# Performance work log

Hardware: AMD Instinct MI355X
Metric: run time of the kernel (lower is better)

Reference implementation:

```python
import jax, jax.numpy as jnp
import numpy as np

EPS_SINK = 0.01   # SinkhornDistance eps
N_ITERS = 20      # fixed iteration count (original: max 100 with host-side early exit)
BN_EPS = 1e-5


def _conv(x, w, b):
    # NCHW 3x3 (or 1x1) conv, SAME padding
    y = jax.lax.conv_general_dilated(x, w, (1, 1), 'SAME',
                                     dimension_numbers=('NCHW', 'OIHW', 'NCHW'))
    return y + b[None, :, None, None]


def _bn_train(x, gamma, beta):
    # BatchNorm2d in training mode: batch statistics over (N,H,W)
    m = jnp.mean(x, axis=(0, 2, 3), keepdims=True)
    v = jnp.var(x, axis=(0, 2, 3), keepdims=True)
    return gamma[None, :, None, None] * (x - m) * jax.lax.rsqrt(v + BN_EPS) + beta[None, :, None, None]


def _calc_mean_std(f, eps=1e-5):
    m = jnp.mean(f, axis=(2, 3), keepdims=True)
    s = jnp.sqrt(jnp.var(f, axis=(2, 3), keepdims=True) + eps)
    return m, s


def _sinkhorn_pi(x, y, eps):
    # x: [b, n, d] content points, y: [b, m, d] style points. Cosine-distance cost.
    xn = x / jnp.linalg.norm(x, axis=-1, keepdims=True)
    yn = y / jnp.linalg.norm(y, axis=-1, keepdims=True)
    C = 1.0 - jnp.einsum('bnd,bmd->bnm', xn, yn)          # [b, n, m]
    b, n, m = C.shape
    log_mu = jnp.log(jnp.full((b, n), 1.0 / n) + 1e-8)
    log_nu = jnp.log(jnp.full((b, m), 1.0 / m) + 1e-8)

    def Mmat(u, v):
        # (-C + u_i + v_j) / eps
        return (-C + u[..., None] + v[..., None, :]) / eps

    def step(carry, _):
        u, v = carry
        u = eps * (log_mu - jax.scipy.special.logsumexp(Mmat(u, v), axis=-1)) + u
        v = eps * (log_nu - jax.scipy.special.logsumexp(Mmat(u, v), axis=-2)) + v
        return (u, v), None

    (u, v), _ = jax.lax.scan(step, (jnp.zeros((b, n)), jnp.zeros((b, m))), None, length=N_ITERS)
    return jnp.exp(Mmat(u, v))                             # transport plan pi


def setup_inputs() -> dict:
    key = jax.random.key(0)
    ks = jax.random.split(key, 16)
    bs, dim, h, w = 4, 512, 32, 32
    s = 0.05
    return {
        'content_feat': jax.random.normal(ks[0], (bs, dim, h, w), jnp.float32),
        'style_feat':   jax.random.normal(ks[1], (bs, dim, h, w), jnp.float32),
        # alpha_predictor (version 1): conv(1024->256,3x3) ReLU BN, conv(256->256,3x3) ReLU BN, conv(256->512,3x3)
        'w1': jax.random.normal(ks[2], (256, 1024, 3, 3), jnp.float32) * s,
        'b1': jnp.zeros((256,), jnp.float32),
        'g1': jnp.ones((256,), jnp.float32),
        'be1': jnp.zeros((256,), jnp.float32),
        'w2': jax.random.normal(ks[3], (256, 256, 3, 3), jnp.float32) * s,
        'b2': jnp.zeros((256,), jnp.float32),
        'g2': jnp.ones((256,), jnp.float32),
        'be2': jnp.zeros((256,), jnp.float32),
        'w3': jax.random.normal(ks[4], (512, 256, 3, 3), jnp.float32) * s,
        'b3': jnp.zeros((512,), jnp.float32),
        # stand-in decoder head: 3x3 conv 512->3 (decoder is an external injected module)
        'dec_w': jax.random.normal(ks[5], (3, 512, 3, 3), jnp.float32) * s,
        'dec_b': jnp.zeros((3,), jnp.float32),
    }


def reference(content_feat, style_feat, w1, b1, g1, be1, w2, b2, g2, be2, w3, b3, dec_w, dec_b):
    bs, dim, h, w = content_feat.shape
    cf = content_feat.reshape(bs, dim, h * w).transpose(0, 2, 1)   # [b, hw, d]
    sf = style_feat.reshape(bs, dim, h * w).transpose(0, 2, 1)
    pi = _sinkhorn_pi(cf, sf, EPS_SINK) * (h * w)                  # style_assign: pi * h * w
    t = jnp.einsum('bnm,bmd->bnd', pi, sf).transpose(0, 2, 1).reshape(bs, dim, h, w)
    cm, cs = _calc_mean_std(content_feat)
    c_normed = (content_feat - cm) / cs
    a = _bn_train(jax.nn.relu(_conv(jnp.concatenate([t, content_feat], axis=1), w1, b1)), g1, be1)
    a = _bn_train(jax.nn.relu(_conv(a, w2, b2)), g2, be2)
    alpha = _conv(a, w3, b3)
    t = alpha * c_normed + t
    g_t = _conv(t, dec_w, dec_b)
    return g_t
```

## Files before the change

### kernel.cpp

```cpp
#include <hip/hip_runtime.h>

typedef unsigned short u16;
typedef unsigned int u32;
typedef unsigned long long u64;
typedef float f32x4 __attribute__((ext_vector_type(4)));
typedef short bf16x8 __attribute__((ext_vector_type(8)));

#define DEV static __device__ __forceinline__

DEV float bf2f(u16 u){ union{float f; u32 i;} x; x.i = ((u32)u) << 16; return x.f; }
DEV u16 f2bf(float f){ union{float f; u32 i;} x; x.f = f; u32 u = x.i;
  return (u16)((u + 0x7fffu + ((u >> 16) & 1u)) >> 16); }
DEV u16 f2h(float f){ _Float16 h = (_Float16)f; u16 u; __builtin_memcpy(&u, &h, 2); return u; }
DEV float h2f(u16 u){ _Float16 h; __builtin_memcpy(&h, &u, 2); return (float)h; }
DEV uint4 pack8(const u16* s){ uint4 v;
  v.x = (u32)s[0] | ((u32)s[1]<<16); v.y = (u32)s[2] | ((u32)s[3]<<16);
  v.z = (u32)s[4] | ((u32)s[5]<<16); v.w = (u32)s[6] | ((u32)s[7]<<16); return v; }
DEV f32x4 mfma16(bf16x8 a, bf16x8 b, f32x4 c){
  return __builtin_amdgcn_mfma_f32_16x16x32_bf16(a, b, c, 0, 0, 0);
}
DEV bf16x8 ldfrag(const u16* p){ return *(const bf16x8*)p; }

DEV void st_agent(float* p, float v){
  __hip_atomic_store(p, v, __ATOMIC_RELAXED, __HIP_MEMORY_SCOPE_AGENT); }
DEV float2 ld_agent2(const float* p){
  u64 u = __hip_atomic_load((const u64*)p, __ATOMIC_RELAXED, __HIP_MEMORY_SCOPE_AGENT);
  union{u64 u; float2 f;} c; c.u = u; return c.f; }
DEV void st_agent_u32(u32* p, u32 v){
  __hip_atomic_store(p, v, __ATOMIC_RELAXED, __HIP_MEMORY_SCOPE_AGENT); }
DEV u32 ld_agent_u32(const u32* p){
  return __hip_atomic_load(p, __ATOMIC_RELAXED, __HIP_MEMORY_SCOPE_AGENT); }

constexpr float SCL = 144.269504088896341f;
constexpr float LOG2MU = -9.99998522680257f;

constexpr size_t MB = 1ull << 20;
constexpr size_t OFF_G    = 0;
constexpr size_t OFF_GT   = 8*MB;
constexpr size_t OFF_U    = 16*MB;
constexpr size_t OFF_V    = OFF_U   + (16<<10);
constexpr size_t OFF_BAR  = OFF_V   + (16<<10);
constexpr size_t OFF_INS  = OFF_BAR + (16<<10);
constexpr size_t OFF_CNM  = OFF_INS + (16<<10);
constexpr size_t OFF_CNIS = OFF_CNM + (8<<10);
constexpr size_t OFF_BNS  = OFF_CNIS+ (8<<10);
constexpr size_t OFF_PNP  = OFF_BNS + (4<<10);
constexpr size_t OFF_CFH  = 17*MB;
constexpr size_t OFF_CFL  = 21*MB;
constexpr size_t OFF_SFH  = 25*MB;
constexpr size_t OFF_SFL  = 29*MB;
constexpr size_t OFF_SNB  = 33*MB;
constexpr size_t OFF_TN   = 37*MB;
constexpr size_t OFF_TCP  = 45*MB;
constexpr size_t OFF_W1P  = 53*MB;
constexpr size_t OFF_W2P  = OFF_W1P + 9*256*1024*2;
constexpr size_t OFF_W3P  = OFF_W2P + 9*256*256*2;
constexpr size_t OFF_WDP  = OFF_W3P + 9*512*256*2;
constexpr size_t OFF_PIP  = 62*MB;
constexpr size_t OFF_Z1  = 17*MB;
constexpr size_t OFF_A1P = 25*MB;
constexpr size_t OFF_Z2  = 27*MB;
constexpr size_t OFF_A2P = 35*MB;
constexpr size_t OFF_T2P = 17*MB;

__global__ void stats_k(const float* __restrict__ cf, const float* __restrict__ sf,
                        float* __restrict__ cnm, float* __restrict__ cnis,
                        float* __restrict__ part, float* __restrict__ zUV,
                        float* __restrict__ zBNS, u32* __restrict__ zbar,
                        const float* __restrict__ w1, const float* __restrict__ w2,
                        const float* __restrict__ w3, const float* __restrict__ wd,
                        u16* __restrict__ w1p, u16* __restrict__ w2p,
                        u16* __restrict__ w3p, u16* __restrict__ wdp){
  int blk = blockIdx.x;
  if (blk < 2048){
    int bd = blk;
    float4 v = ((const float4*)(cf + (size_t)bd*1024))[threadIdx.x];
    float s = v.x+v.y+v.z+v.w;
    float q = v.x*v.x+v.y*v.y+v.z*v.z+v.w*v.w;
    #pragma unroll
    for (int m = 32; m >= 1; m >>= 1){ s += __shfl_xor(s, m, 64); q += __shfl_xor(q, m, 64); }
    __shared__ float ls[4], lq[4];
    int w = threadIdx.x >> 6;
    if ((threadIdx.x & 63) == 0){ ls[w] = s; lq[w] = q; }
    __syncthreads();
    if (threadIdx.x == 0){
      float S = ls[0]+ls[1]+ls[2]+ls[3], Q = lq[0]+lq[1]+lq[2]+lq[3];
      float mean = S * (1.f/1024.f);
      float var  = Q * (1.f/1024.f) - mean*mean;
      cnm[bd] = mean; cnis[bd] = rsqrtf(var + 1e-5f);
    }
    return;
  }
  if (blk < 2304){
    int rel = blk - 2048;
    int x = rel & 15, y = (rel >> 4) & 7, src = rel >> 7;
    const float* in = src ? sf : cf;
    int p = x*256 + threadIdx.x;
    int b = p >> 10, pp = p & 1023;
    const float* base = in + ((size_t)(b*512 + y*64))*1024 + pp;
    float s = 0.f;
    #pragma unroll 8
    for (int d = 0; d < 64; ++d){ float xx = base[(size_t)d*1024]; s += xx*xx; }
    part[((size_t)(src*8 + y))*4096 + p] = s;
    return;
  }
  if (blk < 2336){
    zUV[(blk - 2304)*256 + threadIdx.x] = 0.f;
    return;
  }
  if (blk < 2340){
    zBNS[(blk - 2336)*256 + threadIdx.x] = 0.f;
    return;
  }
  if (blk < 2356){
    zbar[(blk - 2340)*256 + threadIdx.x] = 0u;
    return;
  }
  int pblk = blk - 2356;
  const float* w; u16* wp; int CI, NCK, rel;
  if (pblk < 512){ w = w1; wp = w1p; CI = 1024; NCK = 32; rel = pblk; }
  else if (pblk < 640){ w = w2; wp = w2p; CI = 256; NCK = 8; rel = pblk - 512; }
  else if (pblk < 896){ w = w3; wp = w3p; CI = 256; NCK = 8; rel = pblk - 640; }
  else {
    int o = (pblk - 896)*256 + threadIdx.x;
    int ci = o & 511; int r = o >> 9; int co = r & 15; int tap = r >> 4;
    wdp[o] = f2bf((co < 3) ? wd[(size_t)(co*512 + ci)*9 + tap] : 0.f);
    return;
  }
  int g = rel / NCK, ck = rel % NCK;
  __shared__ float L[16*288];
  const float* base = w + ((size_t)(g*16)*CI + ck*32)*9;
  #pragma unroll
  for (int i = 0; i < 18; ++i){
    int idx = i*256 + threadIdx.x;
    int row = idx / 288, col = idx - row*288;
    L[row*288 + col] = base[(size_t)row*CI*9 + col];
  }
  __syncthreads();
  u16* dst = wp + ((size_t)(g*NCK + ck)*9)*512;
  #pragma unroll
  for (int i = 0; i < 18; ++i){
    int j = i*256 + threadIdx.x;
    int tap = j >> 9, r = j & 511, lane = r >> 3, e = r & 7;
    int co = lane & 15, cil = ((lane >> 4) & 3)*8 + e;
    dst[j] = f2bf(L[co*288 + cil*9 + tap]);
  }
}

__global__ void tsplit_k(const float* __restrict__ cf, const float* __restrict__ sf,
                         const float* __restrict__ pnp,
                         u16* __restrict__ cfh, u16* __restrict__ cfl,
                         u16* __restrict__ sfh, u16* __restrict__ sfl,
                         u16* __restrict__ tcp, u16* __restrict__ snb){
  __shared__ float tile[64][65];
  int z = blockIdx.z, is_style = z >> 2, b = z & 3;
  const float* src = is_style ? sf : cf;
  u16* hi = is_style ? sfh : cfh;
  u16* lo = is_style ? sfl : cfl;
  int p0 = blockIdx.x*64, d0 = blockIdx.y*64;
  int r = threadIdx.x >> 2, c0 = (threadIdx.x & 3) * 16;
  const float* sp = src + ((size_t)(b*512 + d0 + r))*1024 + p0 + c0;
  float v[16];
  #pragma unroll
  for (int e = 0; e < 4; ++e){
    float4 t4 = ((const float4*)sp)[e];
    v[e*4+0]=t4.x; v[e*4+1]=t4.y; v[e*4+2]=t4.z; v[e*4+3]=t4.w;
  }
  #pragma unroll
  for (int j = 0; j < 16; ++j) tile[r][c0+j] = v[j];
  if (is_style){
    u16 t16[16];
    #pragma unroll
    for (int j = 0; j < 16; ++j) t16[j] = f2bf(v[j]);
    uint4* ap = (uint4*)(snb + ((size_t)(b*512 + d0 + r))*1024 + p0 + c0);
    ap[0] = pack8(t16); ap[1] = pack8(t16+8);
  }
  __syncthreads();
  int pr = r, dc0 = c0;
  float inv;
  {
    const float* pp = pnp + (size_t)(is_style ? 8*4096 : 0) + ((b<<10) + p0 + pr);
    float s = 0.f;
    #pragma unroll
    for (int j = 0; j < 8; ++j) s += pp[j*4096];
    inv = rsqrtf(s);
  }
  u16 h16[16], l16[16], t16[16];
  #pragma unroll
  for (int j = 0; j < 16; ++j){
    float x = tile[dc0+j][pr];
    t16[j] = f2bf(x);
    float xn = x * inv;
    u16 h = f2bf(xn);
    h16[j] = h;
    l16[j] = f2bf(xn - bf2f(h));
  }
  size_t orow = (size_t)((b<<10) + p0 + pr);
  uint4* hp = (uint4*)(hi + orow*512 + d0 + dc0);
  uint4* lp = (uint4*)(lo + orow*512 + d0 + dc0);
  hp[0] = pack8(h16); hp[1] = pack8(h16+8);
  lp[0] = pack8(l16); lp[1] = pack8(l16+8);
  if (!is_style){
    int D = d0 + dc0;
    size_t off = ((size_t)(16 + (D>>5))*4096 + orow)*32 + (D&31);
    *(uint4*)(tcp + off)     = pack8(t16);
    *(uint4*)(tcp + off + 8) = pack8(t16+8);
  }
}

__global__ __launch_bounds__(256) void cgemm_k(const u16* __restrict__ cfh, const u16* __restrict__ cfl,
        const u16* __restrict__ sfh, const u16* __restrict__ sfl,
        u16* __restrict__ G, u16* __restrict__ Gt){
  __shared__ __align__(16) u16 SH[4*128*40];
  u16* Ah = SH;          u16* Al = SH + 5120;
  u16* Bh = SH + 10240;  u16* Bl = SH + 15360;
  int b = blockIdx.z;
  size_t abase = ((size_t)((b<<10) + blockIdx.x*128))*512;
  size_t bbase = ((size_t)((b<<10) + blockIdx.y*128))*512;
  int lane = threadIdx.x & 63, wid = threadIdx.x >> 6;
  int wm = (wid >> 1)*64, wn = (wid & 1)*64;
  int fr = lane & 15, qd = lane >> 4;
  int sr = threadIdx.x >> 1, sc = (threadIdx.x & 1)*16;
  const u16 *pA = cfh + abase, *pB = cfl + abase, *pC = sfh + bbase, *pD = sfl + bbase;
  uint4 rA0, rA1, rB0, rB1, rC0, rC1, rD0, rD1;
  auto issue = [&](int kk){
    size_t g0 = (size_t)sr*512 + kk + sc;
    rA0 = *(const uint4*)(pA + g0); rA1 = *(const uint4*)(pA + g0 + 8);
    rB0 = *(const uint4*)(pB + g0); rB1 = *(const uint4*)(pB + g0 + 8);
    rC0 = *(const uint4*)(pC + g0); rC1 = *(const uint4*)(pC + g0 + 8);
    rD0 = *(const uint4*)(pD + g0); rD1 = *(const uint4*)(pD + g0 + 8);
  };
  f32x4 acc[4][4] = {};
  issue(0);
  for (int kk = 0; kk < 512; kk += 32){
    *(uint4*)&Ah[sr*40+sc]   = rA0; *(uint4*)&Ah[sr*40+sc+8] = rA1;
    *(uint4*)&Al[sr*40+sc]   = rB0; *(uint4*)&Al[sr*40+sc+8] = rB1;
    *(uint4*)&Bh[sr*40+sc]   = rC0; *(uint4*)&Bh[sr*40+sc+8] = rC1;
    *(uint4*)&Bl[sr*40+sc]   = rD0; *(uint4*)&Bl[sr*40+sc+8] = rD1;
    __syncthreads();
    if (kk + 32 < 512) issue(kk + 32);
    bf16x8 bhf[4], blf[4];
    #pragma unroll
    for (int ni = 0; ni < 4; ++ni){
      bhf[ni] = ldfrag(&Bh[(wn + ni*16 + fr)*40 + qd*8]);
      blf[ni] = ldfrag(&Bl[(wn + ni*16 + fr)*40 + qd*8]);
    }
    #pragma unroll
    for (int mi = 0; mi < 4; ++mi){
      bf16x8 ah = ldfrag(&Ah[(wm + mi*16 + fr)*40 + qd*8]);
      bf16x8 al = ldfrag(&Al[(wm + mi*16 + fr)*40 + qd*8]);
      #pragma unroll
      for (int ni = 0; ni < 4; ++ni){
        acc[mi][ni] = mfma16(ah, bhf[ni], acc[mi][ni]);
        acc[mi][ni] = mfma16(ah, blf[ni], acc[mi][ni]);
        acc[mi][ni] = mfma16(al, bhf[ni], acc[mi][ni]);
      }
    }
    __syncthreads();
  }
  #pragma unroll
  for (int mi = 0; mi < 4; ++mi)
    #pragma unroll
    for (int ni = 0; ni < 4; ++ni)
      #pragma unroll
      for (int rg = 0; rg < 4; ++rg){
        int r = wm + mi*16 + qd*4 + rg;
        int c = wn + ni*16 + fr;
        SH[r*136 + c] = f2h((acc[mi][ni][rg] - 1.f) * SCL);
      }
  __syncthreads();
  size_t gb = (((size_t)b) << 20) + (size_t)(blockIdx.x*128)*1024 + blockIdx.y*128;
  #pragma unroll
  for (int i = 0; i < 8; ++i){
    int idx = i*256 + threadIdx.x;
    int r = idx >> 4, c4 = idx & 15;
    *(uint4*)(G + gb + (size_t)r*1024 + c4*8) = *(const uint4*)&SH[r*136 + c4*8];
  }
  __syncthreads();
  #pragma unroll
  for (int mi = 0; mi < 4; ++mi)
    #pragma unroll
    for (int ni = 0; ni < 4; ++ni)
      #pragma unroll
      for (int rg = 0; rg < 4; ++rg){
        int r = wm + mi*16 + qd*4 + rg;
        int c = wn + ni*16 + fr;
        SH[c*136 + r] = f2h((acc[mi][ni][rg] - 1.f) * SCL);
      }
  __syncthreads();
  size_t gtb = (((size_t)b) << 20) + (size_t)(blockIdx.y*128)*1024 + blockIdx.x*128;
  #pragma unroll
  for (int i = 0; i < 8; ++i){
    int idx = i*256 + threadIdx.x;
    int r = idx >> 4, c4 = idx & 15;
    *(uint4*)(Gt + gtb + (size_t)r*1024 + c4*8) = *(const uint4*)&SH[r*136 + c4*8];
  }
}

__global__ __launch_bounds__(512) void sink_k(const u16* __restrict__ G, const u16* __restrict__ Gt,
        float* __restrict__ U, float* __restrict__ V,
        u32* __restrict__ flags, u16* __restrict__ pip,
        const u16* __restrict__ cin, const u16* __restrict__ wpk,
        float* __restrict__ z1out){
  __shared__ __align__(16) u16 LL[2][16*1024];
  int blk = blockIdx.x;
  int tid = threadIdx.x;
  if (blk >= 256){
    u16* As = LL[0];
    int cbid = blk - 256;
    int cx = cbid & 15, cy = (cbid >> 4) & 3, b = cbid >> 6;
    const int NCK_TOT = 32, NCK = 16, ck0 = 16;
    int c0 = cy*64, r0 = cx*2;
    int lane = tid & 63, wid = tid >> 6;
    int wm = (wid >> 2)*32, wn = (wid & 3)*16;
    int fr = lane & 15, qd = lane >> 4;
    int hrow = tid >> 2, ah = (tid & 3)*8;
    int gy = r0 - 1 + (hrow >> 5);
    bool a_ok = ((unsigned)gy < 32u);
    size_t arow = (size_t)(b<<10) + (r0-1)*32 + hrow;
    uint4 pa = {0,0,0,0};
    auto issueA = [&](int ck){
      if (a_ok) pa = *(const uint4*)(cin + ((size_t)(ck0+ck)*4096 + arow)*32 + ah);
    };
    int g0 = (c0 + wn) >> 4;
    const u16* wb = wpk + ((size_t)g0*NCK_TOT + ck0)*9*512 + lane*8;
    f32x4 acc[2] = {};
    issueA(0);
    for (int ck = 0; ck < NCK; ++ck){
      *(uint4*)&As[hrow*40 + ah] = pa;
      __syncthreads();
      if (ck + 1 < NCK) issueA(ck + 1);
      #pragma unroll
      for (int tap = 0; tap < 9; ++tap){
        const int dy = tap/3 - 1, dx = tap%3 - 1;
        bf16x8 bf = ldfrag(wb + (size_t)(ck*9 + tap)*512);
        #pragma unroll
        for (int mi = 0; mi < 2; ++mi){
          int p0w = wm + mi*16;
          int pcol = (p0w & 31) + fr + dx;
          int lr = (p0w >> 5) + dy + 1;
          bool okc = (unsigned)pcol < 32u;
          bf16x8 af = ldfrag(&As[(lr*32 + (okc ? pcol : 0))*40 + qd*8]);
          if (!okc) af = bf16x8(0);
          acc[mi] = mfma16(af, bf, acc[mi]);
        }
      }
      __syncthreads();
    }
    #pragma unroll
    for (int mi = 0; mi < 2; ++mi)
      #pragma unroll
      for (int rg = 0; rg < 4; ++rg){
        int pp = cx*64 + wm + mi*16 + qd*4 + rg;
        int cc = c0 + wn + fr;
        size_t ro = (size_t)((b<<10) + pp);
        z1out[(size_t)4096*256 + ro*256 + cc] = acc[mi][rg];
      }
    return;
  }
  int b = blk >> 6;
  int sub = blk & 63;
  int rb = sub << 4;
  size_t gbase = ((size_t)((b << 10) + rb)) << 10;
  {
    const uint4* g0 = (const uint4*)(G + gbase);
    const uint4* g1 = (const uint4*)(Gt + gbase);
    uint4* d0 = (uint4*)LL[0];
    uint4* d1 = (uint4*)LL[1];
    #pragma unroll
    for (int i = 0; i < 4; ++i){
      d0[i*512 + tid] = g0[i*512 + tid];
      d1[i*512 + tid] = g1[i*512 + tid];
    }
  }
  __syncthreads();
  int wid = tid >> 6, lane = tid & 63;
  float* Ub = U + (b << 10);
  float* Vb = V + (b << 10);
  u32* fgrp = flags + (b << 6)*16;
  u32* fmine = fgrp + sub*16;
  int r0 = wid << 1;
  int cbase = lane << 2;
  int budget = 1 << 21;

  float o0 = 0.f, o1 = 0.f;
  auto dopass = [&](int which, const float* __restrict__ inv, float* __restrict__ outv, int tgt){
    float va[16];
    #pragma unroll
    for (int k = 0; k < 4; ++k){
      #pragma unroll
      for (int j = 0; j < 2; ++j){
        float2 t = ld_agent2(inv + k*256 + cbase + j*2);
        va[k*4 + j*2]     = t.x;
        va[k*4 + j*2 + 1] = t.y;
      }
    }
    #pragma unroll
    for (int rr = 0; rr < 2; ++rr){
      int row = r0 + rr;
      float x[16]; float mx = -3.0e38f;
      #pragma unroll
      for (int k = 0; k < 4; ++k){
        uint2 g2 = *(const uint2*)(&LL[which][row*1024 + k*256 + cbase]);
        float t0 = h2f((u16)(g2.x & 0xffffu)) + va[k*4+0];
        float t1 = h2f((u16)(g2.x >> 16))     + va[k*4+1];
        float t2 = h2f((u16)(g2.y & 0xffffu)) + va[k*4+2];
        float t3 = h2f((u16)(g2.y >> 16))     + va[k*4+3];
        x[k*4+0]=t0; x[k*4+1]=t1; x[k*4+2]=t2; x[k*4+3]=t3;
        mx = fmaxf(mx, fmaxf(fmaxf(t0,t1), fmaxf(t2,t3)));
      }
      #pragma unroll
      for (int m = 32; m >= 1; m >>= 1) mx = fmaxf(mx, __shfl_xor(mx, m, 64));
      float s = 0.f;
      #pragma unroll
      for (int i = 0; i < 16; ++i) s += exp2f(x[i] - mx);
      #pragma unroll
      for (int m = 32; m >= 1; m >>= 1) s += __shfl_xor(s, m, 64);
      float o = LOG2MU - (mx + log2f(s));
      if (rr == 0) o0 = o; else o1 = o;
      if (lane == 0) st_agent(outv + rb + row, o);
    }
    __syncthreads();
    if (tid == 0) st_agent_u32(fmine, (u32)tgt);
    if (tid < 64){
      u32* fl = fgrp + tid*16;
      for (;;){
        u32 v = ld_agent_u32(fl);
        if (__all((int)(v >= (u32)tgt))) break;
        if (--budget < 0) break;
        __builtin_amdgcn_s_sleep(1);
      }
    }
    __syncthreads();
  };

  float ku0 = 0.f, ku1 = 0.f;
  for (int it = 0; it < 20; ++it){
    dopass(0, Vb, Ub, 2*it + 1);
    ku0 = o0; ku1 = o1;
    dopass(1, Ub, Vb, 2*it + 2);
  }

  float va[16];
  #pragma unroll
  for (int k = 0; k < 4; ++k){
    #pragma unroll
    for (int j = 0; j < 2; ++j){
      float2 t = ld_agent2(Vb + k*256 + cbase + j*2);
      va[k*4 + j*2]     = t.x;
      va[k*4 + j*2 + 1] = t.y;
    }
  }
  #pragma unroll
  for (int rr = 0; rr < 2; ++rr){
    int row = r0 + rr;
    float ur = (rr == 0 ? ku0 : ku1) + 10.f;
    size_t orow = ((size_t)((b << 10) + rb + row)) << 10;
    #pragma unroll
    for (int k = 0; k < 4; ++k){
      uint2 g2 = *(const uint2*)(&LL[0][row*1024 + k*256 + cbase]);
      u16 o[4];
      o[0] = f2bf(exp2f(h2f((u16)(g2.x & 0xffffu)) + va[k*4+0] + ur));
      o[1] = f2bf(exp2f(h2f((u16)(g2.x >> 16))     + va[k*4+1] + ur));
      o[2] = f2bf(exp2f(h2f((u16)(g2.y & 0xffffu)) + va[k*4+2] + ur));
      o[3] = f2bf(exp2f(h2f((u16)(g2.y >> 16))     + va[k*4+3] + ur));
      uint2 pk; pk.x = (u32)o[0] | ((u32)o[1]<<16); pk.y = (u32)o[2] | ((u32)o[3]<<16);
      *(uint2*)(pip + orow + k*256 + cbase) = pk;
    }
  }
}

__global__ __launch_bounds__(256) void tgemm_k(const u16* __restrict__ pip,
        const u16* __restrict__ snb, float* __restrict__ tn, u16* __restrict__ tcp){
  __shared__ __align__(16) u16 As[64*40], Bs[128*40];
  int b = blockIdx.z, p0 = blockIdx.x*64, d0 = blockIdx.y*128;
  int tid = threadIdx.x, lane = tid & 63, wid = tid >> 6;
  int wm = (wid >> 1)*32, wn = (wid & 1)*64;
  int fr = lane & 15, qd = lane >> 4;
  int a_r = tid >> 2, a_c = (tid & 3)*8;
  int b_r = tid >> 1, b_c = (tid & 1)*16;
  const u16* Arow = pip + (((size_t)((b<<10) + p0 + a_r)) << 10) + a_c;
  const u16* Brow = snb + (((size_t)(b*512 + d0 + b_r)) << 10) + b_c;
  uint4 pa, pb0, pb1;
  auto issue = [&](int kk){
    pa = *(const uint4*)(Arow + kk);
    const uint4* bp = (const uint4*)(Brow + kk);
    pb0 = bp[0]; pb1 = bp[1];
  };
  f32x4 acc[2][4] = {};
  issue(0);
  for (int kk = 0; kk < 1024; kk += 32){
    *(uint4*)&As[a_r*40 + a_c] = pa;
    *(uint4*)&Bs[b_r*40 + b_c] = pb0;
    *(uint4*)&Bs[b_r*40 + b_c + 8] = pb1;
    __syncthreads();
    if (kk + 32 < 1024) issue(kk + 32);
    bf16x8 bfr[4];
    #pragma unroll
    for (int ni = 0; ni < 4; ++ni) bfr[ni] = ldfrag(&Bs[(wn + ni*16 + fr)*40 + qd*8]);
    #pragma unroll
    for (int mi = 0; mi < 2; ++mi){
      bf16x8 afr = ldfrag(&As[(wm + mi*16 + fr)*40 + qd*8]);
      #pragma unroll
      for (int ni = 0; ni < 4; ++ni) acc[mi][ni] = mfma16(afr, bfr[ni], acc[mi][ni]);
    }
    __syncthreads();
  }
  #pragma unroll
  for (int mi = 0; mi < 2; ++mi)
    #pragma unroll
    for (int ni = 0; ni < 4; ++ni)
      #pragma unroll
      for (int rg = 0; rg < 4; ++rg){
        int p = p0 + wm + mi*16 + qd*4 + rg;
        int d = d0 + wn + ni*16 + fr;
        float vout = acc[mi][ni][rg];
        size_t ro = (size_t)((b<<10) + p);
        tn[ro*512 + d] = vout;
        tcp[((size_t)(d>>5)*4096 + ro)*32 + (d&31)] = f2bf(vout);
      }
}

template<int CI, int CO, int KSPLIT, int MODE>
__global__ __launch_bounds__(256) void conv_k(const u16* __restrict__ inp, const u16* __restrict__ wpk,
        const float* __restrict__ bias, float* __restrict__ fout, u16* __restrict__ bout,
        const u16* __restrict__ tcp, const float* __restrict__ cnm, const float* __restrict__ cnis,
        const float* __restrict__ tn){
  constexpr int NCK_TOT = CI/32, NCK = NCK_TOT/KSPLIT;
  __shared__ __align__(16) u16 As[128*40];
  int b = blockIdx.z & 3, ks = blockIdx.z >> 2;
  int c0 = blockIdx.y*64;
  int r0 = blockIdx.x*2;
  int tid = threadIdx.x, lane = tid & 63, wid = tid >> 6;
  int wm = (wid >> 1)*32, wn = (wid & 1)*32;
  int fr = lane & 15, qd = lane >> 4;
  int ck0 = ks*NCK;
  int hrow = tid >> 1;
  int ah = (tid & 1)*16;
  int gy = r0 - 1 + (hrow >> 5);
  bool a_ok = ((unsigned)gy < 32u);
  size_t arow = (size_t)(b<<10) + (r0-1)*32 + hrow;
  uint4 pa0 = {0,0,0,0}, pa1 = {0,0,0,0};
  auto issueA = [&](int ck){
    if (a_ok){
      const uint4* s = (const uint4*)(inp + ((size_t)(ck0+ck)*4096 + arow)*32 + ah);
      pa0 = s[0]; pa1 = s[1];
    }
  };
  int g0 = (c0 + wn) >> 4;
  const u16* wb0 = wpk + ((size_t)(g0    )*NCK_TOT + ck0)*9*512 + lane*8;
  const u16* wb1 = wpk + ((size_t)(g0 + 1)*NCK_TOT + ck0)*9*512 + lane*8;

  f32x4 acc[2][2] = {};
  issueA(0);
  for (int ck = 0; ck < NCK; ++ck){
    *(uint4*)&As[hrow*40 + ah]     = pa0;
    *(uint4*)&As[hrow*40 + ah + 8] = pa1;
    __syncthreads();
    if (ck + 1 < NCK) issueA(ck + 1);
    #pragma unroll
    for (int tap = 0; tap < 9; ++tap){
      const int dy = tap/3 - 1, dx = tap%3 - 1;
      bf16x8 bf0 = ldfrag(wb0 + (size_t)(ck*9 + tap)*512);
      bf16x8 bf1 = ldfrag(wb1 + (size_t)(ck*9 + tap)*512);
      #pragma unroll
      for (int mi = 0; mi < 2; ++mi){
        int p0w = wm + mi*16;
        int pcol = (p0w & 31) + fr + dx;
        int lr = (p0w >> 5) + dy + 1;
        bool okc = (unsigned)pcol < 32u;
        bf16x8 af = ldfrag(&As[(lr*32 + (okc ? pcol : 0))*40 + qd*8]);
        if (!okc) af = bf16x8(0);
        acc[mi][0] = mfma16(af, bf0, acc[mi][0]);
        acc[mi][1] = mfma16(af, bf1, acc[mi][1]);
      }
    }
    __syncthreads();
  }
  #pragma unroll
  for (int mi = 0; mi < 2; ++mi)
    #pragma unroll
    for (int ni = 0; ni < 2; ++ni)
      #pragma unroll
      for (int rg = 0; rg < 4; ++rg){
        int pp = blockIdx.x*64 + wm + mi*16 + qd*4 + rg;
        int cc = c0 + wn + ni*16 + fr;
        float v = acc[mi][ni][rg];
        size_t ro = (size_t)((b<<10) + pp);
        if (MODE == 0){
          fout[(size_t)ks*4096*CO + ro*CO + cc] = v;
        } else {
          float alpha = v + bias[cc];
          float cn = (bf2f(tcp[((size_t)(16 + (cc>>5))*4096 + ro)*32 + (cc&31)])
                      - cnm[(b<<9) + cc]) * cnis[(b<<9) + cc];
          bout[((size_t)(cc>>5)*4096 + ro)*32 + (cc&31)] = f2bf(alpha*cn + tn[ro*512 + cc]);
        }
      }
}

__global__ __launch_bounds__(512) void dec_k(const u16* __restrict__ t2p, const u16* __restrict__ wdp,
                                             const float* __restrict__ db, float* __restrict__ out){
  __shared__ float wlds[3*4608];
  int tid = threadIdx.x;
  for (int k = tid; k < 3*4608; k += 512){
    int c = k / 4608, rem = k - c*4608;
    int tap = rem >> 9, ci = rem & 511;
    wlds[k] = bf2f(wdp[(size_t)(tap*16 + c)*512 + ci]);
  }
  __syncthreads();
  int b = blockIdx.x >> 5;
  int p = ((blockIdx.x & 31) << 5) + (tid >> 4);
  int sub = tid & 15;
  int py = p >> 5, px = p & 31;
  float a0 = 0.f, a1 = 0.f, a2 = 0.f;
  for (int tap = 0; tap < 9; ++tap){
    int sy = py + tap/3 - 1, sx = px + tap%3 - 1;
    if (((unsigned)sy < 32u) && ((unsigned)sx < 32u)){
      size_t row = (size_t)((b<<10) + (sy<<5) + sx);
      const float* w0 = wlds + tap*512;
      #pragma unroll
      for (int j = 0; j < 4; ++j){
        int ci0 = j*128 + sub*8;
        uint4 v = *(const uint4*)(t2p + ((size_t)(ci0>>5)*4096 + row)*32 + (ci0&31));
        u32 ww[4] = {v.x, v.y, v.z, v.w};
        #pragma unroll
        for (int e = 0; e < 8; ++e){
          float x = bf2f((u16)((e & 1) ? (ww[e>>1] >> 16) : (ww[e>>1] & 0xffffu)));
          a0 += x * w0[ci0 + e];
          a1 += x * w0[4608 + ci0 + e];
          a2 += x * w0[9216 + ci0 + e];
        }
      }
    }
  }
  #pragma unroll
  for (int m = 8; m >= 1; m >>= 1){
    a0 += __shfl_xor(a0, m, 64);
    a1 += __shfl_xor(a1, m, 64);
    a2 += __shfl_xor(a2, m, 64);
  }
  if (sub == 0){
    out[((size_t)(b*3 + 0) << 10) + p] = a0 + db[0];
    out[((size_t)(b*3 + 1) << 10) + p] = a1 + db[1];
    out[((size_t)(b*3 + 2) << 10) + p] = a2 + db[2];
  }
}

__global__ void bn_stats_k(const float* __restrict__ z, const float* __restrict__ bias,
                           float* __restrict__ sums){
  int c = blockIdx.x*64 + (threadIdx.x & 63);
  int w = threadIdx.x >> 6;
  int rbase = blockIdx.y*128 + w*32;
  float bi = bias[c];
  float s = 0.f, q = 0.f;
  for (int i = 0; i < 32; ++i){
    size_t ro = (size_t)(rbase + i)*256 + c;
    float x = fmaxf(z[ro] + z[4096*256 + ro] + bi, 0.f);
    s += x; q += x*x;
  }
  __shared__ float ls[4][64], lq[4][64];
  ls[w][threadIdx.x & 63] = s; lq[w][threadIdx.x & 63] = q;
  __syncthreads();
  if (threadIdx.x < 64){
    float S = ls[0][threadIdx.x]+ls[1][threadIdx.x]+ls[2][threadIdx.x]+ls[3][threadIdx.x];
    float Q = lq[0][threadIdx.x]+lq[1][threadIdx.x]+lq[2][threadIdx.x]+lq[3][threadIdx.x];
    atomicAdd(&sums[blockIdx.x*64 + threadIdx.x], S);
    atomicAdd(&sums[256 + blockIdx.x*64 + threadIdx.x], Q);
  }
}

__global__ void bn_apply_k(const float* __restrict__ z, const float* __restrict__ bias,
                           const float* __restrict__ sums, const float* __restrict__ gamma,
                           const float* __restrict__ beta, u16* __restrict__ ap){
  int idx = blockIdx.x*256 + threadIdx.x;
  float4 va = ((const float4*)z)[idx];
  float4 vb = ((const float4*)(z + 4096*256))[idx];
  int row = idx >> 6;
  int cc0 = (idx << 2) & 255;
  float e[4] = {va.x+vb.x, va.y+vb.y, va.z+vb.z, va.w+vb.w};
  u16 o[4];
  #pragma unroll
  for (int k = 0; k < 4; ++k){
    int c = cc0 + k;
    float mean = sums[c] * (1.f/4096.f);
    float var  = sums[256 + c] * (1.f/4096.f) - mean*mean;
    float sc = gamma[c] * rsqrtf(var + 1e-5f);
    float sh = beta[c] - mean*sc;
    float x = fmaxf(e[k] + bias[c], 0.f);
    o[k] = f2bf(x*sc + sh);
  }
  uint2 pk; pk.x = (u32)o[0] | ((u32)o[1]<<16); pk.y = (u32)o[2] | ((u32)o[3]<<16);
  *(uint2*)(ap + ((size_t)(cc0>>5)*4096 + row)*32 + (cc0&31)) = pk;
}

extern "C" void kernel_launch(void* const* d_in, const int* in_sizes, int n_in,
                              void* d_out, int out_size, void* d_ws, size_t ws_size,
                              hipStream_t stream){
  const float* cf  = (const float*)d_in[0];
  const float* sf  = (const float*)d_in[1];
  const float* w1  = (const float*)d_in[2];
  const float* b1  = (const float*)d_in[3];
  const float* g1  = (const float*)d_in[4];
  const float* be1 = (const float*)d_in[5];
  const float* w2  = (const float*)d_in[6];
  const float* b2  = (const float*)d_in[7];
  const float* g2  = (const float*)d_in[8];
  const float* be2 = (const float*)d_in[9];
  const float* w3  = (const float*)d_in[10];
  const float* b3  = (const float*)d_in[11];
  const float* dw  = (const float*)d_in[12];
  const float* db  = (const float*)d_in[13];

  char* ws = (char*)d_ws;
  u16* G    = (u16*)(ws + OFF_G);
  u16* Gt   = (u16*)(ws + OFF_GT);
  float* U    = (float*)(ws + OFF_U);
  float* V    = (float*)(ws + OFF_V);
  u32* bar    = (u32*)(ws + OFF_BAR);
  float* cnm  = (float*)(ws + OFF_CNM);
  float* cnis = (float*)(ws + OFF_CNIS);
  float* bns1 = (float*)(ws + OFF_BNS);
  float* bns2 = bns1 + 512;
  float* pnp  = (float*)(ws + OFF_PNP);
  u16* cfh = (u16*)(ws + OFF_CFH);
  u16* cfl = (u16*)(ws + OFF_CFL);
  u16* sfh = (u16*)(ws + OFF_SFH);
  u16* sfl = (u16*)(ws + OFF_SFL);
  u16* snb = (u16*)(ws + OFF_SNB);
  float* tn  = (float*)(ws + OFF_TN);
  u16* tcp = (u16*)(ws + OFF_TCP);
  u16* w1p = (u16*)(ws + OFF_W1P);
  u16* w2p = (u16*)(ws + OFF_W2P);
  u16* w3p = (u16*)(ws + OFF_W3P);
  u16* wdp = (u16*)(ws + OFF_WDP);
  u16* pip = (u16*)(ws + OFF_PIP);
  float* z1  = (float*)(ws + OFF_Z1);
  u16*   a1p = (u16*)(ws + OFF_A1P);
  float* z2  = (float*)(ws + OFF_Z2);
  u16*   a2p = (u16*)(ws + OFF_A2P);
  u16*   t2p = (u16*)(ws + OFF_T2P);

  stats_k<<<3540, 256, 0, stream>>>(cf, sf, cnm, cnis, pnp, U, bns1, bar,
                                    w1, w2, w3, dw, w1p, w2p, w3p, wdp);
  tsplit_k<<<dim3(16, 8, 8), 256, 0, stream>>>(cf, sf, pnp, cfh, cfl, sfh, sfl, tcp, snb);

  cgemm_k<<<dim3(8, 8, 4), 256, 0, stream>>>(cfh, cfl, sfh, sfl, G, Gt);

  sink_k<<<512, 512, 0, stream>>>(G, Gt, U, V, bar, pip, tcp, w1p, z1);

  tgemm_k<<<dim3(16, 4, 4), 256, 0, stream>>>(pip, snb, tn, tcp);

  conv_k<1024, 256, 2, 0><<<dim3(16, 4, 4), 256, 0, stream>>>(
      tcp, w1p, nullptr, z1, nullptr, nullptr, nullptr, nullptr, nullptr);
  bn_stats_k<<<dim3(4, 32), 256, 0, stream>>>(z1, b1, bns1);
  bn_apply_k<<<1024, 256, 0, stream>>>(z1, b1, bns1, g1, be1, a1p);

  conv_k<256, 256, 2, 0><<<dim3(16, 4, 8), 256, 0, stream>>>(
      a1p, w2p, nullptr, z2, nullptr, nullptr, nullptr, nullptr, nullptr);
  bn_stats_k<<<dim3(4, 32), 256, 0, stream>>>(z2, b2, bns2);
  bn_apply_k<<<1024, 256, 0, stream>>>(z2, b2, bns2, g2, be2, a2p);

  conv_k<256, 512, 1, 1><<<dim3(16, 8, 4), 256, 0, stream>>>(
      a2p, w3p, b3, nullptr, t2p, tcp, cnm, cnis, tn);

  dec_k<<<128, 512, 0, stream>>>(t2p, wdp, db, (float*)d_out);

  (void)in_sizes; (void)n_in; (void)out_size; (void)ws_size;
}
```

Measured before the change: 389.9 us.

## Fuse transport GEMM into Sinkhorn kernel and merge BN stats/apply with grid barrier

After: 400.4 us. 1.03x slower.

```diff
diff --git a/kernel.cpp b/kernel.cpp
--- a/kernel.cpp
+++ b/kernel.cpp
@@ -23,6 +23,8 @@
 
 DEV void st_agent(float* p, float v){
   __hip_atomic_store(p, v, __ATOMIC_RELAXED, __HIP_MEMORY_SCOPE_AGENT); }
+DEV float ld_agentf(const float* p){
+  return __hip_atomic_load(p, __ATOMIC_RELAXED, __HIP_MEMORY_SCOPE_AGENT); }
 DEV float2 ld_agent2(const float* p){
   u64 u = __hip_atomic_load((const u64*)p, __ATOMIC_RELAXED, __HIP_MEMORY_SCOPE_AGENT);
   union{u64 u; float2 f;} c; c.u = u; return c.f; }
@@ -40,8 +42,8 @@
 constexpr size_t OFF_U    = 16*MB;
 constexpr size_t OFF_V    = OFF_U   + (16<<10);
 constexpr size_t OFF_BAR  = OFF_V   + (16<<10);
-constexpr size_t OFF_INS  = OFF_BAR + (16<<10);
-constexpr size_t OFF_CNM  = OFF_INS + (16<<10);
+constexpr size_t OFF_CTR  = OFF_BAR + (16<<10);
+constexpr size_t OFF_CNM  = OFF_CTR + (16<<10);
 constexpr size_t OFF_CNIS = OFF_CNM + (8<<10);
 constexpr size_t OFF_BNS  = OFF_CNIS+ (8<<10);
 constexpr size_t OFF_PNP  = OFF_BNS + (4<<10);
@@ -56,7 +58,6 @@
 constexpr size_t OFF_W2P  = OFF_W1P + 9*256*1024*2;
 constexpr size_t OFF_W3P  = OFF_W2P + 9*256*256*2;
 constexpr size_t OFF_WDP  = OFF_W3P + 9*512*256*2;
-constexpr size_t OFF_PIP  = 62*MB;
 constexpr size_t OFF_Z1  = 17*MB;
 constexpr size_t OFF_A1P = 25*MB;
 constexpr size_t OFF_Z2  = 27*MB;
@@ -67,6 +68,7 @@
                         float* __restrict__ cnm, float* __restrict__ cnis,
                         float* __restrict__ part, float* __restrict__ zUV,
                         float* __restrict__ zBNS, u32* __restrict__ zbar,
+                        u32* __restrict__ zctr,
                         const float* __restrict__ w1, const float* __restrict__ w2,
                         const float* __restrict__ w3, const float* __restrict__ wd,
                         u16* __restrict__ w1p, u16* __restrict__ w2p,
@@ -116,7 +118,11 @@
     zbar[(blk - 2340)*256 + threadIdx.x] = 0u;
     return;
   }
-  int pblk = blk - 2356;
+  if (blk < 2357){
+    zctr[threadIdx.x] = 0u;
+    return;
+  }
+  int pblk = blk - 2357;
   const float* w; u16* wp; int CI, NCK, rel;
   if (pblk < 512){ w = w1; wp = w1p; CI = 1024; NCK = 32; rel = pblk; }
   else if (pblk < 640){ w = w2; wp = w2p; CI = 256; NCK = 8; rel = pblk - 512; }
@@ -299,9 +305,10 @@
 
 __global__ __launch_bounds__(512) void sink_k(const u16* __restrict__ G, const u16* __restrict__ Gt,
         float* __restrict__ U, float* __restrict__ V,
-        u32* __restrict__ flags, u16* __restrict__ pip,
+        u32* __restrict__ flags,
         const u16* __restrict__ cin, const u16* __restrict__ wpk,
-        float* __restrict__ z1out){
+        float* __restrict__ z1out,
+        const u16* __restrict__ snb, float* __restrict__ tn, u16* __restrict__ tcp){
   __shared__ __align__(16) u16 LL[2][16*1024];
   int blk = blockIdx.x;
   int tid = threadIdx.x;
@@ -375,6 +382,7 @@
   }
   __syncthreads();
   int wid = tid >> 6, lane = tid & 63;
+  int fr = lane & 15, qd = lane >> 4;
   float* Ub = U + (b << 10);
   float* Vb = V + (b << 10);
   u32* fgrp = flags + (b << 6)*16;
@@ -441,84 +449,72 @@
     dopass(1, Ub, Vb, 2*it + 2);
   }
 
-  float va[16];
-  #pragma unroll
-  for (int k = 0; k < 4; ++k){
-    #pragma unroll
-    for (int j = 0; j < 2; ++j){
-      float2 t = ld_agent2(Vb + k*256 + cbase + j*2);
-      va[k*4 + j*2]     = t.x;
-      va[k*4 + j*2 + 1] = t.y;
-    }
-  }
-  #pragma unroll
-  for (int rr = 0; rr < 2; ++rr){
-    int row = r0 + rr;
-    float ur = (rr == 0 ? ku0 : ku1) + 10.f;
-    size_t orow = ((size_t)((b << 10) + rb + row)) << 10;
+  {
+    float va[16];
     #pragma unroll
     for (int k = 0; k < 4; ++k){
-      uint2 g2 = *(const uint2*)(&LL[0][row*1024 + k*256 + cbase]);
-      u16 o[4];
-      o[0] = f2bf(exp2f(h2f((u16)(g2.x & 0xffffu)) + va[k*4+0] + ur));
-      o[1] = f2bf(exp2f(h2f((u16)(g2.x >> 16))     + va[k*4+1] + ur));
-      o[2] = f2bf(exp2f(h2f((u16)(g2.y & 0xffffu)) + va[k*4+2] + ur));
-      o[3] = f2bf(exp2f(h2f((u16)(g2.y >> 16))     + va[k*4+3] + ur));
-      uint2 pk; pk.x = (u32)o[0] | ((u32)o[1]<<16); pk.y = (u32)o[2] | ((u32)o[3]<<16);
-      *(uint2*)(pip + orow + k*256 + cbase) = pk;
-    }
-  }
-}
-
-__global__ __launch_bounds__(256) void tgemm_k(const u16* __restrict__ pip,
-        const u16* __restrict__ snb, float* __restrict__ tn, u16* __restrict__ tcp){
-  __shared__ __align__(16) u16 As[64*40], Bs[128*40];
-  int b = blockIdx.z, p0 = blockIdx.x*64, d0 = blockIdx.y*128;
-  int tid = threadIdx.x, lane = tid & 63, wid = tid >> 6;
-  int wm = (wid >> 1)*32, wn = (wid & 1)*64;
-  int fr = lane & 15, qd = lane >> 4;
-  int a_r = tid >> 2, a_c = (tid & 3)*8;
-  int b_r = tid >> 1, b_c = (tid & 1)*16;
-  const u16* Arow = pip + (((size_t)((b<<10) + p0 + a_r)) << 10) + a_c;
-  const u16* Brow = snb + (((size_t)(b*512 + d0 + b_r)) << 10) + b_c;
-  uint4 pa, pb0, pb1;
-  auto issue = [&](int kk){
-    pa = *(const uint4*)(Arow + kk);
-    const uint4* bp = (const uint4*)(Brow + kk);
-    pb0 = bp[0]; pb1 = bp[1];
-  };
-  f32x4 acc[2][4] = {};
-  issue(0);
-  for (int kk = 0; kk < 1024; kk += 32){
-    *(uint4*)&As[a_r*40 + a_c] = pa;
-    *(uint4*)&Bs[b_r*40 + b_c] = pb0;
-    *(uint4*)&Bs[b_r*40 + b_c + 8] = pb1;
-    __syncthreads();
-    if (kk + 32 < 1024) issue(kk + 32);
-    bf16x8 bfr[4];
-    #pragma unroll
-    for (int ni = 0; ni < 4; ++ni) bfr[ni] = ldfrag(&Bs[(wn + ni*16 + fr)*40 + qd*8]);
-    #pragma unroll
-    for (int mi = 0; mi < 2; ++mi){
-      bf16x8 afr = ldfrag(&As[(wm + mi*16 + fr)*40 + qd*8]);
-      #pragma unroll
-      for (int ni = 0; ni < 4; ++ni) acc[mi][ni] = mfma16(afr, bfr[ni], acc[mi][ni]);
-    }
-    __syncthreads();
-  }
-  #pragma unroll
-  for (int mi = 0; mi < 2; ++mi)
-    #pragma unroll
-    for (int ni = 0; ni < 4; ++ni)
+      #pragma unroll
+      for (int j = 0; j < 2; ++j){
+        float2 t = ld_agent2(Vb + k*256 + cbase + j*2);
+        va[k*4 + j*2]     = t.x;
+        va[k*4 + j*2 + 1] = t.y;
+      }
+    }
+    #pragma unroll
+    for (int rr = 0; rr < 2; ++rr){
+      int row = r0 + rr;
+      float ur = (rr == 0 ? ku0 : ku1) + 10.f;
+      int sw = (row & 7) << 3;
+      #pragma unroll
+      for (int k = 0; k < 4; ++k){
+        uint2 g2 = *(const uint2*)(&LL[0][row*1024 + k*256 + cbase]);
+        u16 o[4];
+        o[0] = f2bf(exp2f(h2f((u16)(g2.x & 0xffffu)) + va[k*4+0] + ur));
+        o[1] = f2bf(exp2f(h2f((u16)(g2.x >> 16))     + va[k*4+1] + ur));
+        o[2] = f2bf(exp2f(h2f((u16)(g2.y & 0xffffu)) + va[k*4+2] + ur));
+        o[3] = f2bf(exp2f(h2f((u16)(g2.y >> 16))     + va[k*4+3] + ur));
+        uint2 pk; pk.x = (u32)o[0] | ((u32)o[1]<<16); pk.y = (u32)o[2] | ((u32)o[3]<<16);
+        *(uint2*)(&LL[1][row*1024 + ((k*256 + cbase) ^ sw)]) = pk;
+      }
+    }
+  }
+  __syncthreads();
+  {
+    int d0w = wid << 6;
+    const u16* Bb = snb + (((size_t)(b*512 + d0w)) << 10);
+    f32x4 tac[4] = {};
+    uint4 pb0, pb1, pb2, pb3;
+    auto issueB = [&](int ks){
+      int off = ks*32 + qd*8;
+      pb0 = *(const uint4*)(Bb + (((size_t)(     fr)) << 10) + off);
+      pb1 = *(const uint4*)(Bb + (((size_t)(16 + fr)) << 10) + off);
+      pb2 = *(const uint4*)(Bb + (((size_t)(32 + fr)) << 10) + off);
+      pb3 = *(const uint4*)(Bb + (((size_t)(48 + fr)) << 10) + off);
+    };
+    issueB(0);
+    int asw = (fr & 7) << 3;
+    for (int ks = 0; ks < 32; ++ks){
+      union{uint4 u; bf16x8 v;} c0_, c1_, c2_, c3_;
+      c0_.u = pb0; c1_.u = pb1; c2_.u = pb2; c3_.u = pb3;
+      if (ks + 1 < 32) issueB(ks + 1);
+      bf16x8 af = ldfrag(&LL[1][fr*1024 + ((ks*32 + qd*8) ^ asw)]);
+      tac[0] = mfma16(af, c0_.v, tac[0]);
+      tac[1] = mfma16(af, c1_.v, tac[1]);
+      tac[2] = mfma16(af, c2_.v, tac[2]);
+      tac[3] = mfma16(af, c3_.v, tac[3]);
+    }
+    #pragma unroll
+    for (int t = 0; t < 4; ++t)
       #pragma unroll
       for (int rg = 0; rg < 4; ++rg){
-        int p = p0 + wm + mi*16 + qd*4 + rg;
-        int d = d0 + wn + ni*16 + fr;
-        float vout = acc[mi][ni][rg];
-        size_t ro = (size_t)((b<<10) + p);
-        tn[ro*512 + d] = vout;
-        tcp[((size_t)(d>>5)*4096 + ro)*32 + (d&31)] = f2bf(vout);
-      }
+        int p = qd*4 + rg;
+        int d = d0w + t*16 + fr;
+        size_t ro = (size_t)((b<<10) + rb + p);
+        float v = tac[t][rg];
+        tn[ro*512 + d] = v;
+        tcp[((size_t)(d>>5)*4096 + ro)*32 + (d&31)] = f2bf(v);
+      }
+  }
 }
 
 template<int CI, int CO, int KSPLIT, int MODE>
@@ -646,51 +642,39 @@
   }
 }
 
-__global__ void bn_stats_k(const float* __restrict__ z, const float* __restrict__ bias,
-                           float* __restrict__ sums){
-  int c = blockIdx.x*64 + (threadIdx.x & 63);
-  int w = threadIdx.x >> 6;
-  int rbase = blockIdx.y*128 + w*32;
+__global__ __launch_bounds__(256) void bn_k(const float* __restrict__ z, const float* __restrict__ bias,
+                    float* __restrict__ sums, const float* __restrict__ gamma,
+                    const float* __restrict__ beta, u16* __restrict__ ap,
+                    u32* __restrict__ ctr){
+  int c = threadIdx.x;
+  int r0 = blockIdx.x*32;
   float bi = bias[c];
+  float xv[32];
   float s = 0.f, q = 0.f;
+  #pragma unroll
   for (int i = 0; i < 32; ++i){
-    size_t ro = (size_t)(rbase + i)*256 + c;
-    float x = fmaxf(z[ro] + z[4096*256 + ro] + bi, 0.f);
-    s += x; q += x*x;
-  }
-  __shared__ float ls[4][64], lq[4][64];
-  ls[w][threadIdx.x & 63] = s; lq[w][threadIdx.x & 63] = q;
-  __syncthreads();
-  if (threadIdx.x < 64){
-    float S = ls[0][threadIdx.x]+ls[1][threadIdx.x]+ls[2][threadIdx.x]+ls[3][threadIdx.x];
-    float Q = lq[0][threadIdx.x]+lq[1][threadIdx.x]+lq[2][threadIdx.x]+lq[3][threadIdx.x];
-    atomicAdd(&sums[blockIdx.x*64 + threadIdx.x], S);
-    atomicAdd(&sums[256 + blockIdx.x*64 + threadIdx.x], Q);
-  }
-}
-
-__global__ void bn_apply_k(const float* __restrict__ z, const float* __restrict__ bias,
-                           const float* __restrict__ sums, const float* __restrict__ gamma,
-                           const float* __restrict__ beta, u16* __restrict__ ap){
-  int idx = blockIdx.x*256 + threadIdx.x;
-  float4 va = ((const float4*)z)[idx];
-  float4 vb = ((const float4*)(z + 4096*256))[idx];
-  int row = idx >> 6;
-  int cc0 = (idx << 2) & 255;
-  float e[4] = {va.x+vb.x, va.y+vb.y, va.z+vb.z, va.w+vb.w};
-  u16 o[4];
-  #pragma unroll
-  for (int k = 0; k < 4; ++k){
-    int c = cc0 + k;
-    float mean = sums[c] * (1.f/4096.f);
-    float var  = sums[256 + c] * (1.f/4096.f) - mean*mean;
-    float sc = gamma[c] * rsqrtf(var + 1e-5f);
-    float sh = beta[c] - mean*sc;
-    float x = fmaxf(e[k] + bias[c], 0.f);
-    o[k] = f2bf(x*sc + sh);
-  }
-  uint2 pk; pk.x = (u32)o[0] | ((u32)o[1]<<16); pk.y = (u32)o[2] | ((u32)o[3]<<16);
-  *(uint2*)(ap + ((size_t)(cc0>>5)*4096 + row)*32 + (cc0&31)) = pk;
+    size_t ro = (size_t)(r0 + i)*256 + c;
+    float x = fmaxf(z[ro] + z[(size_t)4096*256 + ro] + bi, 0.f);
+    xv[i] = x; s += x; q += x*x;
+  }
+  atomicAdd(&sums[c], s);
+  atomicAdd(&sums[256 + c], q);
+  __syncthreads();
+  if (c == 0){
+    __hip_atomic_fetch_add(ctr, 1u, __ATOMIC_RELAXED, __HIP_MEMORY_SCOPE_AGENT);
+    int budget = 1 << 21;
+    while (ld_agent_u32(ctr) < 128u && --budget > 0) __builtin_amdgcn_s_sleep(1);
+  }
+  __syncthreads();
+  float S = ld_agentf(&sums[c]), Q = ld_agentf(&sums[256 + c]);
+  float mean = S * (1.f/4096.f);
+  float var  = Q * (1.f/4096.f) - mean*mean;
+  float sc = gamma[c] * rsqrtf(var + 1e-5f);
+  float sh = beta[c] - mean*sc;
+  u16* apc = ap + ((size_t)(c>>5)*4096)*32 + (c&31);
+  #pragma unroll
+  for (int i = 0; i < 32; ++i)
+    apc[(size_t)(r0 + i)*32] = f2bf(xv[i]*sc + sh);
 }
 
 extern "C" void kernel_launch(void* const* d_in, const int* in_sizes, int n_in,
@@ -717,6 +701,7 @@
   float* U    = (float*)(ws + OFF_U);
   float* V    = (float*)(ws + OFF_V);
   u32* bar    = (u32*)(ws + OFF_BAR);
+  u32* ctr    = (u32*)(ws + OFF_CTR);
   float* cnm  = (float*)(ws + OFF_CNM);
   float* cnis = (float*)(ws + OFF_CNIS);
   float* bns1 = (float*)(ws + OFF_BNS);
@@ -733,32 +718,27 @@
   u16* w2p = (u16*)(ws + OFF_W2P);
   u16* w3p = (u16*)(ws + OFF_W3P);
   u16* wdp = (u16*)(ws + OFF_WDP);
-  u16* pip = (u16*)(ws + OFF_PIP);
   float* z1  = (float*)(ws + OFF_Z1);
   u16*   a1p = (u16*)(ws + OFF_A1P);
   float* z2  = (float*)(ws + OFF_Z2);
   u16*   a2p = (u16*)(ws + OFF_A2P);
   u16*   t2p = (u16*)(ws + OFF_T2P);
 
-  stats_k<<<3540, 256, 0, stream>>>(cf, sf, cnm, cnis, pnp, U, bns1, bar,
+  stats_k<<<3541, 256, 0, stream>>>(cf, sf, cnm, cnis, pnp, U, bns1, bar, ctr,
                                     w1, w2, w3, dw, w1p, w2p, w3p, wdp);
   tsplit_k<<<dim3(16, 8, 8), 256, 0, stream>>>(cf, sf, pnp, cfh, cfl, sfh, sfl, tcp, snb);
 
   cgemm_k<<<dim3(8, 8, 4), 256, 0, stream>>>(cfh, cfl, sfh, sfl, G, Gt);
 
-  sink_k<<<512, 512, 0, stream>>>(G, Gt, U, V, bar, pip, tcp, w1p, z1);
-
-  tgemm_k<<<dim3(16, 4, 4), 256, 0, stream>>>(pip, snb, tn, tcp);
+  sink_k<<<512, 512, 0, stream>>>(G, Gt, U, V, bar, tcp, w1p, z1, snb, tn, tcp);
 
   conv_k<1024, 256, 2, 0><<<dim3(16, 4, 4), 256, 0, stream>>>(
       tcp, w1p, nullptr, z1, nullptr, nullptr, nullptr, nullptr, nullptr);
-  bn_stats_k<<<dim3(4, 32), 256, 0, stream>>>(z1, b1, bns1);
-  bn_apply_k<<<1024, 256, 0, stream>>>(z1, b1, bns1, g1, be1, a1p);
+  bn_k<<<128, 256, 0, stream>>>(z1, b1, bns1, g1, be1, a1p, ctr);
 
   conv_k<256, 256, 2, 0><<<dim3(16, 4, 8), 256, 0, stream>>>(
       a1p, w2p, nullptr, z2, nullptr, nullptr, nullptr, nullptr, nullptr);
-  bn_stats_k<<<dim3(4, 32), 256, 0, stream>>>(z2, b2, bns2);
-  bn_apply_k<<<1024, 256, 0, stream>>>(z2, b2, bns2, g2, be2, a2p);
+  bn_k<<<128, 256, 0, stream>>>(z2, b2, bns2, g2, be2, a2p, ctr + 16);
 
   conv_k<256, 512, 1, 1><<<dim3(16, 8, 4), 256, 0, stream>>>(
       a2p, w3p, b3, nullptr, t2p, tcp, cnm, cnis, tn);
```

## Fuse BatchNorm stats and apply into one kernel with a grid barrier

Applied to the files above, without the earlier changes.

Measured after the change: 389.5 us. About the same (-0.1%).

```diff
diff --git a/kernel.cpp b/kernel.cpp
--- a/kernel.cpp
+++ b/kernel.cpp
@@ -23,6 +23,8 @@
 
 DEV void st_agent(float* p, float v){
   __hip_atomic_store(p, v, __ATOMIC_RELAXED, __HIP_MEMORY_SCOPE_AGENT); }
+DEV float ld_agentf(const float* p){
+  return __hip_atomic_load(p, __ATOMIC_RELAXED, __HIP_MEMORY_SCOPE_AGENT); }
 DEV float2 ld_agent2(const float* p){
   u64 u = __hip_atomic_load((const u64*)p, __ATOMIC_RELAXED, __HIP_MEMORY_SCOPE_AGENT);
   union{u64 u; float2 f;} c; c.u = u; return c.f; }
@@ -40,8 +42,8 @@
 constexpr size_t OFF_U    = 16*MB;
 constexpr size_t OFF_V    = OFF_U   + (16<<10);
 constexpr size_t OFF_BAR  = OFF_V   + (16<<10);
-constexpr size_t OFF_INS  = OFF_BAR + (16<<10);
-constexpr size_t OFF_CNM  = OFF_INS + (16<<10);
+constexpr size_t OFF_CTR  = OFF_BAR + (16<<10);
+constexpr size_t OFF_CNM  = OFF_CTR + (16<<10);
 constexpr size_t OFF_CNIS = OFF_CNM + (8<<10);
 constexpr size_t OFF_BNS  = OFF_CNIS+ (8<<10);
 constexpr size_t OFF_PNP  = OFF_BNS + (4<<10);
@@ -67,6 +69,7 @@
                         float* __restrict__ cnm, float* __restrict__ cnis,
                         float* __restrict__ part, float* __restrict__ zUV,
                         float* __restrict__ zBNS, u32* __restrict__ zbar,
+                        u32* __restrict__ zctr,
                         const float* __restrict__ w1, const float* __restrict__ w2,
                         const float* __restrict__ w3, const float* __restrict__ wd,
                         u16* __restrict__ w1p, u16* __restrict__ w2p,
@@ -116,7 +119,11 @@
     zbar[(blk - 2340)*256 + threadIdx.x] = 0u;
     return;
   }
-  int pblk = blk - 2356;
+  if (blk < 2357){
+    zctr[threadIdx.x] = 0u;
+    return;
+  }
+  int pblk = blk - 2357;
   const float* w; u16* wp; int CI, NCK, rel;
   if (pblk < 512){ w = w1; wp = w1p; CI = 1024; NCK = 32; rel = pblk; }
   else if (pblk < 640){ w = w2; wp = w2p; CI = 256; NCK = 8; rel = pblk - 512; }
@@ -646,51 +653,39 @@
   }
 }
 
-__global__ void bn_stats_k(const float* __restrict__ z, const float* __restrict__ bias,
-                           float* __restrict__ sums){
-  int c = blockIdx.x*64 + (threadIdx.x & 63);
-  int w = threadIdx.x >> 6;
-  int rbase = blockIdx.y*128 + w*32;
+__global__ __launch_bounds__(256) void bn_k(const float* __restrict__ z, const float* __restrict__ bias,
+                    float* __restrict__ sums, const float* __restrict__ gamma,
+                    const float* __restrict__ beta, u16* __restrict__ ap,
+                    u32* __restrict__ ctr){
+  int c = threadIdx.x;
+  int r0 = blockIdx.x*32;
   float bi = bias[c];
+  float xv[32];
   float s = 0.f, q = 0.f;
+  #pragma unroll
   for (int i = 0; i < 32; ++i){
-    size_t ro = (size_t)(rbase + i)*256 + c;
-    float x = fmaxf(z[ro] + z[4096*256 + ro] + bi, 0.f);
-    s += x; q += x*x;
-  }
-  __shared__ float ls[4][64], lq[4][64];
-  ls[w][threadIdx.x & 63] = s; lq[w][threadIdx.x & 63] = q;
-  __syncthreads();
-  if (threadIdx.x < 64){
-    float S = ls[0][threadIdx.x]+ls[1][threadIdx.x]+ls[2][threadIdx.x]+ls[3][threadIdx.x];
-    float Q = lq[0][threadIdx.x]+lq[1][threadIdx.x]+lq[2][threadIdx.x]+lq[3][threadIdx.x];
-    atomicAdd(&sums[blockIdx.x*64 + threadIdx.x], S);
-    atomicAdd(&sums[256 + blockIdx.x*64 + threadIdx.x], Q);
-  }
-}
-
-__global__ void bn_apply_k(const float* __restrict__ z, const float* __restrict__ bias,
-                           const float* __restrict__ sums, const float* __restrict__ gamma,
-                           const float* __restrict__ beta, u16* __restrict__ ap){
-  int idx = blockIdx.x*256 + threadIdx.x;
-  float4 va = ((const float4*)z)[idx];
-  float4 vb = ((const float4*)(z + 4096*256))[idx];
-  int row = idx >> 6;
-  int cc0 = (idx << 2) & 255;
-  float e[4] = {va.x+vb.x, va.y+vb.y, va.z+vb.z, va.w+vb.w};
-  u16 o[4];
-  #pragma unroll
-  for (int k = 0; k < 4; ++k){
-    int c = cc0 + k;
-    float mean = sums[c] * (1.f/4096.f);
-    float var  = sums[256 + c] * (1.f/4096.f) - mean*mean;
-    float sc = gamma[c] * rsqrtf(var + 1e-5f);
-    float sh = beta[c] - mean*sc;
-    float x = fmaxf(e[k] + bias[c], 0.f);
-    o[k] = f2bf(x*sc + sh);
-  }
-  uint2 pk; pk.x = (u32)o[0] | ((u32)o[1]<<16); pk.y = (u32)o[2] | ((u32)o[3]<<16);
-  *(uint2*)(ap + ((size_t)(cc0>>5)*4096 + row)*32 + (cc0&31)) = pk;
+    size_t ro = (size_t)(r0 + i)*256 + c;
+    float x = fmaxf(z[ro] + z[(size_t)4096*256 + ro] + bi, 0.f);
+    xv[i] = x; s += x; q += x*x;
+  }
+  atomicAdd(&sums[c], s);
+  atomicAdd(&sums[256 + c], q);
+  __syncthreads();
+  if (c == 0){
+    __hip_atomic_fetch_add(ctr, 1u, __ATOMIC_RELAXED, __HIP_MEMORY_SCOPE_AGENT);
+    int budget = 1 << 21;
+    while (ld_agent_u32(ctr) < 128u && --budget > 0) __builtin_amdgcn_s_sleep(1);
+  }
+  __syncthreads();
+  float S = ld_agentf(&sums[c]), Q = ld_agentf(&sums[256 + c]);
+  float mean = S * (1.f/4096.f);
+  float var  = Q * (1.f/4096.f) - mean*mean;
+  float sc = gamma[c] * rsqrtf(var + 1e-5f);
+  float sh = beta[c] - mean*sc;
+  u16* apc = ap + ((size_t)(c>>5)*4096)*32 + (c&31);
+  #pragma unroll
+  for (int i = 0; i < 32; ++i)
+    apc[(size_t)(r0 + i)*32] = f2bf(xv[i]*sc + sh);
 }
 
 extern "C" void kernel_launch(void* const* d_in, const int* in_sizes, int n_in,
@@ -717,6 +712,7 @@
   float* U    = (float*)(ws + OFF_U);
   float* V    = (float*)(ws + OFF_V);
   u32* bar    = (u32*)(ws + OFF_BAR);
+  u32* ctr    = (u32*)(ws + OFF_CTR);
   float* cnm  = (float*)(ws + OFF_CNM);
   float* cnis = (float*)(ws + OFF_CNIS);
   float* bns1 = (float*)(ws + OFF_BNS);
@@ -740,7 +736,7 @@
   u16*   a2p = (u16*)(ws + OFF_A2P);
   u16*   t2p = (u16*)(ws + OFF_T2P);
 
-  stats_k<<<3540, 256, 0, stream>>>(cf, sf, cnm, cnis, pnp, U, bns1, bar,
+  stats_k<<<3541, 256, 0, stream>>>(cf, sf, cnm, cnis, pnp, U, bns1, bar, ctr,
                                     w1, w2, w3, dw, w1p, w2p, w3p, wdp);
   tsplit_k<<<dim3(16, 8, 8), 256, 0, stream>>>(cf, sf, pnp, cfh, cfl, sfh, sfl, tcp, snb);
 
@@ -752,13 +748,11 @@
 
   conv_k<1024, 256, 2, 0><<<dim3(16, 4, 4), 256, 0, stream>>>(
       tcp, w1p, nullptr, z1, nullptr, nullptr, nullptr, nullptr, nullptr);
-  bn_stats_k<<<dim3(4, 32), 256, 0, stream>>>(z1, b1, bns1);
-  bn_apply_k<<<1024, 256, 0, stream>>>(z1, b1, bns1, g1, be1, a1p);
+  bn_k<<<128, 256, 0, stream>>>(z1, b1, bns1, g1, be1, a1p, ctr);
 
   conv_k<256, 256, 2, 0><<<dim3(16, 4, 8), 256, 0, stream>>>(
       a1p, w2p, nullptr, z2, nullptr, nullptr, nullptr, nullptr, nullptr);
-  bn_stats_k<<<dim3(4, 32), 256, 0, stream>>>(z2, b2, bns2);
-  bn_apply_k<<<1024, 256, 0, stream>>>(z2, b2, bns2, g2, be2, a2p);
+  bn_k<<<128, 256, 0, stream>>>(z2, b2, bns2, g2, be2, a2p, ctr + 16);
 
   conv_k<256, 512, 1, 1><<<dim3(16, 8, 4), 256, 0, stream>>>(
       a2p, w3p, b3, nullptr, t2p, tcp, cnm, cnis, tn);
```
